# Kernel tuning notes

Measured on AMD Instinct MI355X. Metric: run time of the kernel, lower is better.

## Reference

```python
import jax, jax.numpy as jnp
import numpy as np

D_MODEL = 1024
N_HEADS = 16
HEAD_DIM = 64
T = 4096
ROT = HEAD_DIM // 2          # 32 channels get rotary
PAIR = ROT // 2              # 16 cos/sin frequencies
EPS = 1e-6
SCALE = 0.12                 # constant attention scale (not 1/sqrt(d))
ROPE_BASE = 10000.0
VOCAB = 50257


def setup_inputs() -> dict:
    key = jax.random.key(0)
    k_x, k_qkv, k_o, k_tok = jax.random.split(key, 4)
    bound = 0.5 / np.sqrt(D_MODEL)
    x = jax.random.normal(k_x, (1, T, D_MODEL), dtype=jnp.float32)
    w_qkv = jax.random.uniform(k_qkv, (3 * D_MODEL, D_MODEL), jnp.float32, -bound, bound)
    # module uses zero_init for w_o; use small random so output is non-trivial
    w_o = jax.random.uniform(k_o, (D_MODEL, D_MODEL), jnp.float32, -bound, bound)
    q_norm_w = jnp.ones((HEAD_DIM,), jnp.float32)
    k_norm_w = jnp.ones((HEAD_DIM,), jnp.float32)
    tokens = jax.random.randint(k_tok, (1, T), 0, VOCAB, dtype=jnp.int64)
    pos = jnp.arange(T, dtype=jnp.int64)
    # RotaryCache: inv_freq over pair dims, cos/sin of t * inv_freq
    inv_freq = 1.0 / (ROPE_BASE ** (jnp.arange(PAIR, dtype=jnp.float32) / PAIR))
    freqs = jnp.arange(T, dtype=jnp.float32)[:, None] * inv_freq[None, :]  # [T, PAIR]
    return {
        "x": x, "tokens": tokens, "pos": pos,
        "w_qkv": w_qkv, "w_o": w_o,
        "q_norm_w": q_norm_w, "k_norm_w": k_norm_w,
        "cos": jnp.cos(freqs), "sin": jnp.sin(freqs),
        "window_tokens": 1024, "block_size": 128,
    }


def _rmsnorm(x, w):
    var = jnp.mean(x * x, axis=-1, keepdims=True)
    return x * jax.lax.rsqrt(var + EPS) * w


def reference(x, tokens, pos, w_qkv, w_o, q_norm_w, k_norm_w, cos, sin,
              window_tokens, block_size):
    B, Tq, C = x.shape
    H, Dh = N_HEADS, HEAD_DIM
    qkv = x @ w_qkv.T                                  # [B, T, 3C]
    q, k, v = jnp.split(qkv, 3, axis=-1)

    def to_bhtd(t):
        return t.reshape(B, Tq, H, Dh).transpose(0, 2, 1, 3)
    q, k, v = to_bhtd(q), to_bhtd(k), to_bhtd(v)

    q = _rmsnorm(q, q_norm_w)
    k = _rmsnorm(k, k_norm_w)

    # half-truncated RoPE: rotate first ROT channels pairwise (even/odd)
    c = cos[pos][None, None]                           # [1,1,T,PAIR]
    s = sin[pos][None, None]

    def rope_rotate(t):
        t1, t2 = t[..., :ROT], t[..., ROT:]
        even, odd = t1[..., 0::2], t1[..., 1::2]
        r_even = even * c - odd * s
        r_odd = even * s + odd * c
        t1r = jnp.stack([r_even, r_odd], axis=-1).reshape(t1.shape)
        return jnp.concatenate([t1r, t2], axis=-1)

    q = rope_rotate(q)
    k = rope_rotate(k)

    v = v * 0.5                                        # no value-embed branch

    scores = jnp.einsum('bhtd,bhsd->bhts', q, k) * SCALE
    idx = jnp.arange(Tq)
    diff = idx[:, None] - idx[None, :]
    allowed = (diff >= 0) & (diff < window_tokens)     # sliding causal window
    scores = jnp.where(allowed, scores, -jnp.inf)
    p = jax.nn.softmax(scores, axis=-1)
    out = jnp.einsum('bhts,bhsd->bhtd', p, v)
    out = out.transpose(0, 2, 1, 3).reshape(B, Tq, C)
    return out @ w_o.T
```

## Files before the change

### kernel.cpp

```cpp
#include <hip/hip_runtime.h>


typedef __bf16 bf16x8 __attribute__((ext_vector_type(8)));
typedef __bf16 bf16x2 __attribute__((ext_vector_type(2)));
typedef float f32x4 __attribute__((ext_vector_type(4)));
typedef unsigned short u16x8 __attribute__((ext_vector_type(8)));
typedef unsigned short u16x4 __attribute__((ext_vector_type(4)));

#define MFMA16(a, b, c) __builtin_amdgcn_mfma_f32_16x16x32_bf16((a), (b), (c), 0, 0, 0)

__device__ __forceinline__ unsigned short f2bf(float f) {
    unsigned int u = __float_as_uint(f);
    u += 0x7fffu + ((u >> 16) & 1u);
    return (unsigned short)(u >> 16);
}
__device__ __forceinline__ float bf2f(unsigned short h) {
    return __uint_as_float(((unsigned int)h) << 16);
}
__device__ __forceinline__ unsigned int pk2bf(float a, float b) {
#if __has_builtin(__builtin_amdgcn_cvt_pk_bf16_f32)
    bf16x2 v = __builtin_amdgcn_cvt_pk_bf16_f32(a, b);
    return __builtin_bit_cast(unsigned int, v);
#else
    return (unsigned int)f2bf(a) | ((unsigned int)f2bf(b) << 16);
#endif
}
__device__ __forceinline__ float fexp2(float x) {
#if __has_builtin(__builtin_amdgcn_exp2f)
    return __builtin_amdgcn_exp2f(x);
#else
    return exp2f(x);
#endif
}
__device__ __forceinline__ bf16x8 ones_bf16x8() {
    u16x8 u;
#pragma unroll
    for (int j = 0; j < 8; ++j) u[j] = 0x3F80;
    return __builtin_bit_cast(bf16x8, u);
}

__device__ __forceinline__ void gl_lds16(const void* g, void* l) {
    typedef __attribute__((address_space(1))) unsigned int GU;
    typedef __attribute__((address_space(3))) unsigned int LU;
    __builtin_amdgcn_global_load_lds((GU*)(unsigned long long)g,
                                     (LU*)(unsigned int)(unsigned long long)l,
                                     16, 0, 0);
}

__device__ __forceinline__ void wait_vm0() {
    asm volatile("s_waitcnt vmcnt(0)" ::: "memory");
}

__global__ void cvt3_kernel(const float* __restrict__ x,
                            const float* __restrict__ wqkv,
                            const float* __restrict__ wo,
                            unsigned short* __restrict__ xb,
                            unsigned short* __restrict__ wqkvb,
                            unsigned short* __restrict__ wob) {
    int i = blockIdx.x * 256 + threadIdx.x;
    const float* src;
    unsigned short* dst;
    int off;
    if (i < 1048576) { src = x; dst = xb; off = i; }
    else if (i < 1835008) { src = wqkv; dst = wqkvb; off = i - 1048576; }
    else { src = wo; dst = wob; off = i - 1835008; }
    float4 f = ((const float4*)src)[off];
    u16x4 o;
    o[0] = f2bf(f.x); o[1] = f2bf(f.y); o[2] = f2bf(f.z); o[3] = f2bf(f.w);
    ((u16x4*)dst)[off] = o;
}

#define TBS 72
__global__ __launch_bounds__(256, 3) void gemm_qkv(
    const unsigned short* __restrict__ A,
    const unsigned short* __restrict__ Bt,
    const float* __restrict__ cosb, const float* __restrict__ sinb,
    const float* __restrict__ qw, const float* __restrict__ kw,
    unsigned short* __restrict__ Qb,
    unsigned short* __restrict__ Kb,
    unsigned short* __restrict__ Vt)
{
    __shared__ unsigned short smem[16384];
    unsigned short* As0 = smem;
    unsigned short* As1 = smem + 4096;
    unsigned short* Bs0 = smem + 8192;
    unsigned short* Bs1 = smem + 12288;

    const int tid = threadIdx.x;
    const int wave = tid >> 6, lane = tid & 63;
    const int quad = lane >> 4, l16 = lane & 15;
    const int m0 = blockIdx.x * 128, n0 = blockIdx.y * 128;
    const int wm = (wave >> 1) * 64, wn = (wave & 1) * 64;

    f32x4 acc[4][4];
#pragma unroll
    for (int i = 0; i < 4; ++i)
#pragma unroll
        for (int j = 0; j < 4; ++j) acc[i][j] = (f32x4){0.f, 0.f, 0.f, 0.f};

    const int lrow = lane >> 2;
    const int lcol = ((lane & 3) ^ ((lane >> 3) & 3)) * 8;
    const int csw  = (quad ^ ((l16 >> 1) & 3)) * 8;

    for (int k0 = 0; k0 < 1024; k0 += 64) {
        {
            const unsigned short* ab = A + (size_t)(m0 + wave * 16 + lrow) * 1024 + k0 + lcol;
            gl_lds16(ab,              &As0[wave * 512]);
            gl_lds16(ab + 32,         &As1[wave * 512]);
            gl_lds16(ab + 65536,      &As0[2048 + wave * 512]);
            gl_lds16(ab + 65536 + 32, &As1[2048 + wave * 512]);
            const unsigned short* bb = Bt + (size_t)(n0 + wave * 16 + lrow) * 1024 + k0 + lcol;
            gl_lds16(bb,              &Bs0[wave * 512]);
            gl_lds16(bb + 32,         &Bs1[wave * 512]);
            gl_lds16(bb + 65536,      &Bs0[2048 + wave * 512]);
            gl_lds16(bb + 65536 + 32, &Bs1[2048 + wave * 512]);
        }
        __syncthreads();
        {
            bf16x8 af[4], bfr[4];
#pragma unroll
            for (int mt = 0; mt < 4; ++mt)
                af[mt] = *(const bf16x8*)&As0[(wm + mt * 16 + l16) * 32 + csw];
#pragma unroll
            for (int nt = 0; nt < 4; ++nt)
                bfr[nt] = *(const bf16x8*)&Bs0[(wn + nt * 16 + l16) * 32 + csw];
#pragma unroll
            for (int mt = 0; mt < 4; ++mt)
#pragma unroll
                for (int nt = 0; nt < 4; ++nt)
                    acc[mt][nt] = MFMA16(af[mt], bfr[nt], acc[mt][nt]);
        }
        {
            bf16x8 af[4], bfr[4];
#pragma unroll
            for (int mt = 0; mt < 4; ++mt)
                af[mt] = *(const bf16x8*)&As1[(wm + mt * 16 + l16) * 32 + csw];
#pragma unroll
            for (int nt = 0; nt < 4; ++nt)
                bfr[nt] = *(const bf16x8*)&Bs1[(wn + nt * 16 + l16) * 32 + csw];
#pragma unroll
            for (int mt = 0; mt < 4; ++mt)
#pragma unroll
                for (int nt = 0; nt < 4; ++nt)
                    acc[mt][nt] = MFMA16(af[mt], bfr[nt], acc[mt][nt]);
        }
        __syncthreads();
    }

    unsigned short* tbw = smem + wave * 1152;
    const int region = blockIdx.y >> 3;
    const int h = ((blockIdx.y & 7) << 1) + (wave & 1);

    if (region < 2) {
        const float* wgt = region ? kw : qw;
        unsigned short* dst = region ? Kb : Qb;
        const float post = region ? 1.f : 0.17312340490667046f;
        float w[4];
#pragma unroll
        for (int nt = 0; nt < 4; ++nt) w[nt] = wgt[nt * 16 + l16] * post;
#pragma unroll
        for (int mt = 0; mt < 4; ++mt) {
#pragma unroll
            for (int r = 0; r < 4; ++r) {
                const int row = m0 + wm + mt * 16 + quad * 4 + r;
                float ss = 0.f;
#pragma unroll
                for (int nt = 0; nt < 4; ++nt)
                    ss += acc[mt][nt][r] * acc[mt][nt][r];
                ss += __shfl_xor(ss, 1); ss += __shfl_xor(ss, 2);
                ss += __shfl_xor(ss, 4); ss += __shfl_xor(ss, 8);
                const float rn = rsqrtf(ss * (1.f / 64.f) + 1e-6f);
                float val[4];
#pragma unroll
                for (int nt = 0; nt < 4; ++nt)
                    val[nt] = acc[mt][nt][r] * rn * w[nt];
#pragma unroll
                for (int nt = 0; nt < 2; ++nt) {
                    const float prt = __shfl_xor(val[nt], 1);
                    const int p = nt * 8 + (l16 >> 1);
                    const float c = cosb[row * 16 + p];
                    const float s = sinb[row * 16 + p];
                    val[nt] = (l16 & 1) ? (prt * s + val[nt] * c)
                                        : (val[nt] * c - prt * s);
                }
#pragma unroll
                for (int nt = 0; nt < 4; ++nt)
                    tbw[(quad * 4 + r) * TBS + nt * 16 + l16] = f2bf(val[nt]);
            }
            const int t = lane >> 2, dcol = (lane & 3) * 16;
            u16x8 v0 = *(const u16x8*)&tbw[t * TBS + dcol];
            u16x8 v1 = *(const u16x8*)&tbw[t * TBS + dcol + 8];
            const size_t ob = ((size_t)h * 4096 + (m0 + wm + mt * 16 + t)) * 64 + dcol;
            *(u16x8*)&dst[ob] = v0;
            *(u16x8*)&dst[ob + 8] = v1;
        }
    } else {
#pragma unroll
        for (int mt = 0; mt < 4; ++mt) {
#pragma unroll
            for (int nt = 0; nt < 4; ++nt)
#pragma unroll
                for (int r = 0; r < 4; ++r)
                    tbw[(nt * 16 + l16) * 16 + quad * 4 + r] =
                        f2bf(acc[mt][nt][r] * 0.5f);
            const size_t vo = ((size_t)h * 64 + lane) * 4096 + m0 + wm;
#pragma unroll
            for (int q = 0; q < 4; ++q) {
                u16x4 vq = *(const u16x4*)&tbw[lane * 16 + q * 4];
                *(u16x4*)&Vt[vo + q * 16 + mt * 4] = vq;
            }
        }
    }
}

#define PSTR 72

template <int MASK>
__device__ __forceinline__ void qk_exp_2g(
    int sb, int qt0w, int quad, int l16, int csw, int rbase,
    const unsigned short* KsA, const unsigned short* KsB,
    unsigned short* Pw, const bf16x8 (&qf)[2][2])
{
    uint2 hold[2];
#pragma unroll
    for (int i = 0; i < 4; ++i) {
        const bf16x8 kf0 = *(const bf16x8*)&KsA[(rbase + i * 16 + l16) * 32 + csw];
        const bf16x8 kf1 = *(const bf16x8*)&KsB[(rbase + i * 16 + l16) * 32 + csw];
#pragma unroll
        for (int g = 0; g < 2; ++g) {
            f32x4 z = (f32x4){0.f, 0.f, 0.f, 0.f};
            z = MFMA16(kf0, qf[g][0], z);
            z = MFMA16(kf1, qf[g][1], z);
            float p[4];
#pragma unroll
            for (int r = 0; r < 4; ++r) {
                float e = fexp2(z[r]);
                if (MASK) {
                    const int s = sb + i * 16 + quad * 4 + r;
                    e = ((unsigned)((qt0w + g * 16 + l16) - s) < 1024u) ? e : 0.f;
                }
                p[r] = e;
            }
            uint2 pk;
            pk.x = pk2bf(p[0], p[1]);
            pk.y = pk2bf(p[2], p[3]);
            if (i == 0 || i == 2) {
                hold[g] = pk;
            } else {
                uint4 w4;
                w4.x = hold[g].x; w4.y = hold[g].y; w4.z = pk.x; w4.w = pk.y;
                *(uint4*)&Pw[(g * 16 + l16) * PSTR + quad * 16 + (i == 3 ? 8 : 0)] = w4;
            }
        }
    }
}

__device__ __forceinline__ void pv_acc_2g(
    int quad, int l16, int csw,
    const unsigned short* VsA, const unsigned short* VsB,
    const unsigned short* Pw, f32x4 (&o)[2][4], f32x4 (&ls)[2])
{
    bf16x8 pf0[2], pf1[2];
#pragma unroll
    for (int g = 0; g < 2; ++g) {
        pf0[g] = *(const bf16x8*)&Pw[(g * 16 + l16) * PSTR + quad * 8];
        pf1[g] = *(const bf16x8*)&Pw[(g * 16 + l16) * PSTR + 32 + quad * 8];
    }
    const bf16x8 ones = ones_bf16x8();
    __builtin_amdgcn_s_setprio(1);
#pragma unroll
    for (int g = 0; g < 2; ++g) {
        ls[g] = MFMA16(pf0[g], ones, ls[g]);
        ls[g] = MFMA16(pf1[g], ones, ls[g]);
    }
#pragma unroll
    for (int dt = 0; dt < 4; ++dt) {
        const bf16x8 vf0 = *(const bf16x8*)&VsA[(dt * 16 + l16) * 32 + csw];
        const bf16x8 vf1 = *(const bf16x8*)&VsB[(dt * 16 + l16) * 32 + csw];
#pragma unroll
        for (int g = 0; g < 2; ++g) {
            o[g][dt] = MFMA16(pf0[g], vf0, o[g][dt]);
            o[g][dt] = MFMA16(pf1[g], vf1, o[g][dt]);
        }
    }
    __builtin_amdgcn_s_setprio(0);
}

__global__ __launch_bounds__(256) void attn_kernel(
    const unsigned short* __restrict__ Qb,
    const unsigned short* __restrict__ Kb,
    const unsigned short* __restrict__ Vt,
    unsigned short* __restrict__ att)
{
    __shared__ unsigned short KsA[2][4096], KsB[2][4096];
    __shared__ unsigned short Vs0[2048], Vs1[2048];
    __shared__ unsigned short Vs2[2048], Vs3[2048];
    __shared__ unsigned short P[4][32 * PSTR];

    const int bid = blockIdx.x;
    const int h = ((bid & 7) << 1) | ((bid >> 3) & 1);
    const int t0 = (31 - (bid >> 4)) * 128;

    const int tid = threadIdx.x;
    const int wave = tid >> 6, lane = tid & 63;
    const int quad = lane >> 4, l16 = lane & 15;
    const int qt0 = t0 + wave * 32;
    const int srow = lane >> 2;
    const int scol = ((lane & 3) ^ ((lane >> 3) & 3)) * 8;
    const int csw  = (quad ^ ((l16 >> 1) & 3)) * 8;

    const unsigned short* Qh = Qb + (size_t)h * 4096 * 64;
    const unsigned short* Kh = Kb + (size_t)h * 4096 * 64;
    const unsigned short* Vh = Vt + (size_t)h * 64 * 4096;

    bf16x8 qf[2][2];
#pragma unroll
    for (int g = 0; g < 2; ++g) {
        qf[g][0] = *(const bf16x8*)&Qh[(qt0 + g * 16 + l16) * 64 + quad * 8];
        qf[g][1] = *(const bf16x8*)&Qh[(qt0 + g * 16 + l16) * 64 + 32 + quad * 8];
    }

    f32x4 o[2][4];
    f32x4 ls[2];
#pragma unroll
    for (int g = 0; g < 2; ++g) {
        ls[g] = (f32x4){0.f, 0.f, 0.f, 0.f};
#pragma unroll
        for (int dt = 0; dt < 4; ++dt) o[g][dt] = (f32x4){0.f, 0.f, 0.f, 0.f};
    }
    unsigned short* Pw = P[wave];

    auto stageK = [&](int b, int s) {
        if (wave < 2) {
#pragma unroll
            for (int l = 0; l < 4; ++l) {
                const int rg = wave * 4 + l;
                const unsigned short* kb =
                    Kh + (size_t)(s + rg * 16 + srow) * 64 + scol;
                gl_lds16(kb,      &KsA[b][rg * 512]);
                gl_lds16(kb + 32, &KsB[b][rg * 512]);
            }
        }
    };
    auto stageV = [&](int s) {
        if (wave >= 2) {
            const int w2 = wave - 2;
#pragma unroll
            for (int l = 0; l < 2; ++l) {
                const int dg = w2 * 2 + l;
                const unsigned short* vb =
                    Vh + (size_t)(dg * 16 + srow) * 4096 + s + scol;
                gl_lds16(vb,      &Vs0[dg * 512]);
                gl_lds16(vb + 32, &Vs1[dg * 512]);
                gl_lds16(vb + 64, &Vs2[dg * 512]);
                gl_lds16(vb + 96, &Vs3[dg * 512]);
            }
        }
    };

    const int s_lo = (t0 >= 1024) ? (t0 - 1024) : 0;
    const int NT = ((t0 - s_lo) >> 7) + 1;

    stageK(0, s_lo);
    if (wave < 2) wait_vm0();
    __builtin_amdgcn_s_barrier();
    __builtin_amdgcn_sched_barrier(0);
    int buf = 0;
    for (int n = 0; n < NT; ++n) {
        const int s0 = s_lo + n * 128;
        const int sb1 = s0 + 64;
        if (n + 1 < NT) stageK(buf ^ 1, s0 + 128);
        stageV(s0);
        const bool d0 = (s0 + 63 < qt0 - 1023);
        const bool c0 = (s0 + 63 <= qt0) && (s0 >= qt0 - 992);
        const bool d1 = (sb1 > qt0 + 31) || (sb1 + 63 < qt0 - 1023);
        const bool c1 = (sb1 + 63 <= qt0) && (sb1 >= qt0 - 992);
        if (!d0) {
            if (c0) qk_exp_2g<0>(s0, qt0, quad, l16, csw, 0, KsA[buf], KsB[buf],
                                 Pw, qf);
            else    qk_exp_2g<1>(s0, qt0, quad, l16, csw, 0, KsA[buf], KsB[buf],
                                 Pw, qf);
        }
        if (wave >= 2) wait_vm0();
        __builtin_amdgcn_s_barrier();
        __builtin_amdgcn_sched_barrier(0);
        if (!d0) pv_acc_2g(quad, l16, csw, Vs0, Vs1, Pw, o, ls);
        if (!d1) {
            if (c1) qk_exp_2g<0>(sb1, qt0, quad, l16, csw, 64, KsA[buf], KsB[buf],
                                 Pw, qf);
            else    qk_exp_2g<1>(sb1, qt0, quad, l16, csw, 64, KsA[buf], KsB[buf],
                                 Pw, qf);
            pv_acc_2g(quad, l16, csw, Vs2, Vs3, Pw, o, ls);
        }
        if (wave < 2) wait_vm0();
        __builtin_amdgcn_s_barrier();
        __builtin_amdgcn_sched_barrier(0);
        buf ^= 1;
    }

#pragma unroll
    for (int g = 0; g < 2; ++g) {
        float lr[4];
#pragma unroll
        for (int r = 0; r < 4; ++r) lr[r] = 1.f / ls[g][r];
#pragma unroll
        for (int dt = 0; dt < 4; ++dt)
#pragma unroll
            for (int r = 0; r < 4; ++r)
                att[(size_t)(qt0 + g * 16 + quad * 4 + r) * 1024 +
                    h * 64 + dt * 16 + l16] = f2bf(o[g][dt][r] * lr[r]);
    }
}

__global__ __launch_bounds__(256) void gemm_out(
    const unsigned short* __restrict__ A,
    const unsigned short* __restrict__ Bt,
    float* __restrict__ C)
{
    __shared__ unsigned short As0[2][2048], As1[2][2048];
    __shared__ unsigned short Bs0[2][4096], Bs1[2][4096];
    const int tid = threadIdx.x;
    const int wave = tid >> 6, lane = tid & 63;
    const int quad = lane >> 4, l16 = lane & 15;
    const int m0 = blockIdx.x * 64, n0 = blockIdx.y * 128;
    const int wm = (wave >> 1) * 32, wn = (wave & 1) * 64;
    const int lrow = lane >> 2;
    const int lcol = ((lane & 3) ^ ((lane >> 3) & 3)) * 8;
    const int csw  = (quad ^ ((l16 >> 1) & 3)) * 8;

    f32x4 acc[2][4];
#pragma unroll
    for (int i = 0; i < 2; ++i)
#pragma unroll
        for (int j = 0; j < 4; ++j) acc[i][j] = (f32x4){0.f, 0.f, 0.f, 0.f};

    auto stage = [&](int buf, int k0) {
        const unsigned short* ab = A + (size_t)(m0 + wave * 16 + lrow) * 1024 + k0 + lcol;
        gl_lds16(ab,      &As0[buf][wave * 512]);
        gl_lds16(ab + 32, &As1[buf][wave * 512]);
#pragma unroll
        for (int i = 0; i < 2; ++i) {
            const int c = wave * 2 + i;
            const unsigned short* bb = Bt + (size_t)(n0 + c * 16 + lrow) * 1024 + k0 + lcol;
            gl_lds16(bb,      &Bs0[buf][c * 512]);
            gl_lds16(bb + 32, &Bs1[buf][c * 512]);
        }
    };

    stage(0, 0);
    __syncthreads();
    int buf = 0;
    for (int k0 = 0; k0 < 1024; k0 += 64) {
        if (k0 + 64 < 1024) stage(buf ^ 1, k0 + 64);
        {
            bf16x8 af[2], bfr[4];
#pragma unroll
            for (int mt = 0; mt < 2; ++mt)
                af[mt] = *(const bf16x8*)&As0[buf][(wm + mt * 16 + l16) * 32 + csw];
#pragma unroll
            for (int nt = 0; nt < 4; ++nt)
                bfr[nt] = *(const bf16x8*)&Bs0[buf][(wn + nt * 16 + l16) * 32 + csw];
#pragma unroll
            for (int mt = 0; mt < 2; ++mt)
#pragma unroll
                for (int nt = 0; nt < 4; ++nt)
                    acc[mt][nt] = MFMA16(af[mt], bfr[nt], acc[mt][nt]);
        }
        {
            bf16x8 af[2], bfr[4];
#pragma unroll
            for (int mt = 0; mt < 2; ++mt)
                af[mt] = *(const bf16x8*)&As1[buf][(wm + mt * 16 + l16) * 32 + csw];
#pragma unroll
            for (int nt = 0; nt < 4; ++nt)
                bfr[nt] = *(const bf16x8*)&Bs1[buf][(wn + nt * 16 + l16) * 32 + csw];
#pragma unroll
            for (int mt = 0; mt < 2; ++mt)
#pragma unroll
                for (int nt = 0; nt < 4; ++nt)
                    acc[mt][nt] = MFMA16(af[mt], bfr[nt], acc[mt][nt]);
        }
        __syncthreads();
        buf ^= 1;
    }
#pragma unroll
    for (int mt = 0; mt < 2; ++mt)
#pragma unroll
        for (int nt = 0; nt < 4; ++nt)
#pragma unroll
            for (int r = 0; r < 4; ++r) {
                const int row = m0 + wm + mt * 16 + quad * 4 + r;
                const int col = n0 + wn + nt * 16 + l16;
                C[(size_t)row * 1024 + col] = acc[mt][nt][r];
            }
}

extern "C" void kernel_launch(void* const* d_in, const int* in_sizes, int n_in,
                              void* d_out, int out_size, void* d_ws, size_t ws_size,
                              hipStream_t stream) {
    const float* x    = (const float*)d_in[0];
    const float* wqkv = (const float*)d_in[3];
    const float* wo   = (const float*)d_in[4];
    const float* qw   = (const float*)d_in[5];
    const float* kw   = (const float*)d_in[6];
    const float* cosb = (const float*)d_in[7];
    const float* sinb = (const float*)d_in[8];

    char* ws = (char*)d_ws;
    if (ws_size < (size_t)48 * 1024 * 1024) return;
    unsigned short* xb    = (unsigned short*)(ws + ((size_t)0 << 20));
    unsigned short* wqkvb = (unsigned short*)(ws + ((size_t)8 << 20));
    unsigned short* wob   = (unsigned short*)(ws + ((size_t)14 << 20));
    unsigned short* Qb    = (unsigned short*)(ws + ((size_t)16 << 20));
    unsigned short* Kb    = (unsigned short*)(ws + ((size_t)24 << 20));
    unsigned short* Vt    = (unsigned short*)(ws + ((size_t)32 << 20));
    unsigned short* attb  = (unsigned short*)(ws + ((size_t)40 << 20));

    cvt3_kernel<<<8192, 256, 0, stream>>>(x, wqkv, wo, xb, wqkvb, wob);

    gemm_qkv<<<dim3(32, 24), 256, 0, stream>>>(xb, wqkvb, cosb, sinb, qw, kw,
                                               Qb, Kb, Vt);

    attn_kernel<<<512, 256, 0, stream>>>(Qb, Kb, Vt, attb);

    gemm_out<<<dim3(64, 8), 256, 0, stream>>>(attb, wob, (float*)d_out);
}
```

Measured before the change: 173.3 us.

## Load V fragments directly from global into registers, drop V LDS staging

Removes the shared-memory staging of V tiles and the mid-iteration barrier. Each wave now loads its V MFMA fragments straight from global memory into registers before the QK/exp step. K staging is redistributed across all four waves instead of two. This cuts LDS traffic and one barrier per iteration, but every wave now reads V redundantly from global/L2 with strided rows, so the loads may be exposed to latency.

After: 183.6 us. 6.0% more time.

```diff
diff --git a/kernel.cpp b/kernel.cpp
--- a/kernel.cpp
+++ b/kernel.cpp
@@ -256,8 +256,7 @@
 }
 
 __device__ __forceinline__ void pv_acc_2g(
-    int quad, int l16, int csw,
-    const unsigned short* VsA, const unsigned short* VsB,
+    int quad, int l16, const bf16x8 (&vf)[4][2],
     const unsigned short* Pw, f32x4 (&o)[2][4], f32x4 (&ls)[2])
 {
     bf16x8 pf0[2], pf1[2];
@@ -274,15 +273,12 @@
         ls[g] = MFMA16(pf1[g], ones, ls[g]);
     }
 #pragma unroll
-    for (int dt = 0; dt < 4; ++dt) {
-        const bf16x8 vf0 = *(const bf16x8*)&VsA[(dt * 16 + l16) * 32 + csw];
-        const bf16x8 vf1 = *(const bf16x8*)&VsB[(dt * 16 + l16) * 32 + csw];
+    for (int dt = 0; dt < 4; ++dt)
 #pragma unroll
         for (int g = 0; g < 2; ++g) {
-            o[g][dt] = MFMA16(pf0[g], vf0, o[g][dt]);
-            o[g][dt] = MFMA16(pf1[g], vf1, o[g][dt]);
-        }
-    }
+            o[g][dt] = MFMA16(pf0[g], vf[dt][0], o[g][dt]);
+            o[g][dt] = MFMA16(pf1[g], vf[dt][1], o[g][dt]);
+        }
     __builtin_amdgcn_s_setprio(0);
 }
 
@@ -293,8 +289,6 @@
     unsigned short* __restrict__ att)
 {
     __shared__ unsigned short KsA[2][4096], KsB[2][4096];
-    __shared__ unsigned short Vs0[2048], Vs1[2048];
-    __shared__ unsigned short Vs2[2048], Vs3[2048];
     __shared__ unsigned short P[4][32 * PSTR];
 
     const int bid = blockIdx.x;
@@ -331,30 +325,13 @@
     unsigned short* Pw = P[wave];
 
     auto stageK = [&](int b, int s) {
-        if (wave < 2) {
-#pragma unroll
-            for (int l = 0; l < 4; ++l) {
-                const int rg = wave * 4 + l;
-                const unsigned short* kb =
-                    Kh + (size_t)(s + rg * 16 + srow) * 64 + scol;
-                gl_lds16(kb,      &KsA[b][rg * 512]);
-                gl_lds16(kb + 32, &KsB[b][rg * 512]);
-            }
-        }
-    };
-    auto stageV = [&](int s) {
-        if (wave >= 2) {
-            const int w2 = wave - 2;
-#pragma unroll
-            for (int l = 0; l < 2; ++l) {
-                const int dg = w2 * 2 + l;
-                const unsigned short* vb =
-                    Vh + (size_t)(dg * 16 + srow) * 4096 + s + scol;
-                gl_lds16(vb,      &Vs0[dg * 512]);
-                gl_lds16(vb + 32, &Vs1[dg * 512]);
-                gl_lds16(vb + 64, &Vs2[dg * 512]);
-                gl_lds16(vb + 96, &Vs3[dg * 512]);
-            }
+#pragma unroll
+        for (int l = 0; l < 2; ++l) {
+            const int rg = l * 4 + wave;
+            const unsigned short* kb =
+                Kh + (size_t)(s + rg * 16 + srow) * 64 + scol;
+            gl_lds16(kb,      &KsA[b][rg * 512]);
+            gl_lds16(kb + 32, &KsB[b][rg * 512]);
         }
     };
 
@@ -362,7 +339,7 @@
     const int NT = ((t0 - s_lo) >> 7) + 1;
 
     stageK(0, s_lo);
-    if (wave < 2) wait_vm0();
+    wait_vm0();
     __builtin_amdgcn_s_barrier();
     __builtin_amdgcn_sched_barrier(0);
     int buf = 0;
@@ -370,29 +347,39 @@
         const int s0 = s_lo + n * 128;
         const int sb1 = s0 + 64;
         if (n + 1 < NT) stageK(buf ^ 1, s0 + 128);
-        stageV(s0);
         const bool d0 = (s0 + 63 < qt0 - 1023);
         const bool c0 = (s0 + 63 <= qt0) && (s0 >= qt0 - 992);
         const bool d1 = (sb1 > qt0 + 31) || (sb1 + 63 < qt0 - 1023);
         const bool c1 = (sb1 + 63 <= qt0) && (sb1 >= qt0 - 992);
         if (!d0) {
+            bf16x8 vf[4][2];
+            const unsigned short* Vg = Vh + s0;
+#pragma unroll
+            for (int dt = 0; dt < 4; ++dt) {
+                vf[dt][0] = *(const bf16x8*)&Vg[(size_t)(dt * 16 + l16) * 4096 + quad * 8];
+                vf[dt][1] = *(const bf16x8*)&Vg[(size_t)(dt * 16 + l16) * 4096 + 32 + quad * 8];
+            }
             if (c0) qk_exp_2g<0>(s0, qt0, quad, l16, csw, 0, KsA[buf], KsB[buf],
                                  Pw, qf);
             else    qk_exp_2g<1>(s0, qt0, quad, l16, csw, 0, KsA[buf], KsB[buf],
                                  Pw, qf);
-        }
-        if (wave >= 2) wait_vm0();
-        __builtin_amdgcn_s_barrier();
-        __builtin_amdgcn_sched_barrier(0);
-        if (!d0) pv_acc_2g(quad, l16, csw, Vs0, Vs1, Pw, o, ls);
+            pv_acc_2g(quad, l16, vf, Pw, o, ls);
+        }
         if (!d1) {
+            bf16x8 vf[4][2];
+            const unsigned short* Vg = Vh + sb1;
+#pragma unroll
+            for (int dt = 0; dt < 4; ++dt) {
+                vf[dt][0] = *(const bf16x8*)&Vg[(size_t)(dt * 16 + l16) * 4096 + quad * 8];
+                vf[dt][1] = *(const bf16x8*)&Vg[(size_t)(dt * 16 + l16) * 4096 + 32 + quad * 8];
+            }
             if (c1) qk_exp_2g<0>(sb1, qt0, quad, l16, csw, 64, KsA[buf], KsB[buf],
                                  Pw, qf);
             else    qk_exp_2g<1>(sb1, qt0, quad, l16, csw, 64, KsA[buf], KsB[buf],
                                  Pw, qf);
-            pv_acc_2g(quad, l16, csw, Vs2, Vs3, Pw, o, ls);
-        }
-        if (wave < 2) wait_vm0();
+            pv_acc_2g(quad, l16, vf, Pw, o, ls);
+        }
+        wait_vm0();
         __builtin_amdgcn_s_barrier();
         __builtin_amdgcn_sched_barrier(0);
         buf ^= 1;
```
